# Optimization experiments

Measured on AMD Instinct MI355X. Metric: run time of the kernel, lower is better.

Reference implementation:

```python
import jax, jax.numpy as jnp
import numpy as np
import math

N_HEADS = 16
D_EMBED = 1024
D_CROSS = 768
FF_DIM = 4096
D_HEAD = D_EMBED // N_HEADS
LN_EPS = 1e-5


def layer_norm(h, g, b):
    mu = jnp.mean(h, axis=-1, keepdims=True)
    var = jnp.var(h, axis=-1, keepdims=True)
    return (h - mu) * jax.lax.rsqrt(var + LN_EPS) * g + b


def mha(q, k, v):
    # q: [B,Sq,D], k/v: [B,Skv,D] -> split heads, attend, merge
    B, Sq, _ = q.shape
    Skv = k.shape[1]
    qh = q.reshape(B, Sq, N_HEADS, D_HEAD).transpose(0, 2, 1, 3)
    kh = k.reshape(B, Skv, N_HEADS, D_HEAD).transpose(0, 2, 1, 3)
    vh = v.reshape(B, Skv, N_HEADS, D_HEAD).transpose(0, 2, 1, 3)
    scores = jnp.einsum('bhqd,bhkd->bhqk', qh, kh) / math.sqrt(D_HEAD)
    attn = jax.nn.softmax(scores, axis=-1)
    out = jnp.einsum('bhqk,bhkd->bhqd', attn, vh)
    return out.transpose(0, 2, 1, 3).reshape(B, Sq, D_EMBED)


def setup_inputs() -> dict:
    key = jax.random.key(0)
    ks = jax.random.split(key, 24)
    s = 0.02
    inp = {
        'x': jax.random.normal(ks[0], (4, 1024, D_EMBED), jnp.float32),
        'y': jax.random.normal(ks[1], (4, 77, D_CROSS), jnp.float32),
        # self-attention in_proj (d_embed -> 3*d_embed) and out_proj
        'w_qkv': jax.random.normal(ks[2], (D_EMBED, 3 * D_EMBED), jnp.float32) * s,
        'b_qkv': jnp.zeros((3 * D_EMBED,), jnp.float32),
        'w_so': jax.random.normal(ks[3], (D_EMBED, D_EMBED), jnp.float32) * s,
        'b_so': jnp.zeros((D_EMBED,), jnp.float32),
        # cross-attention projections
        'w_q': jax.random.normal(ks[4], (D_EMBED, D_EMBED), jnp.float32) * s,
        'b_q': jnp.zeros((D_EMBED,), jnp.float32),
        'w_k': jax.random.normal(ks[5], (D_CROSS, D_EMBED), jnp.float32) * s,
        'b_k': jnp.zeros((D_EMBED,), jnp.float32),
        'w_v': jax.random.normal(ks[6], (D_CROSS, D_EMBED), jnp.float32) * s,
        'b_v': jnp.zeros((D_EMBED,), jnp.float32),
        'w_co': jax.random.normal(ks[7], (D_EMBED, D_EMBED), jnp.float32) * s,
        'b_co': jnp.zeros((D_EMBED,), jnp.float32),
        # 3-layer FFN
        'w1': jax.random.normal(ks[8], (D_EMBED, FF_DIM), jnp.float32) * s,
        'b1': jnp.zeros((FF_DIM,), jnp.float32),
        'w2': jax.random.normal(ks[9], (FF_DIM, FF_DIM), jnp.float32) * s,
        'b2': jnp.zeros((FF_DIM,), jnp.float32),
        'w3': jax.random.normal(ks[10], (FF_DIM, D_EMBED), jnp.float32) * s,
        'b3': jnp.zeros((D_EMBED,), jnp.float32),
        # single shared LayerNorm (used 3 times, as in the torch module)
        'ln_g': jnp.ones((D_EMBED,), jnp.float32),
        'ln_b': jnp.zeros((D_EMBED,), jnp.float32),
    }
    return inp


def reference(x, y, w_qkv, b_qkv, w_so, b_so, w_q, b_q, w_k, b_k, w_v, b_v,
              w_co, b_co, w1, b1, w2, b2, w3, b3, ln_g, ln_b):
    # --- self attention (no causal mask) ---
    qkv = x @ w_qkv + b_qkv
    q, k, v = jnp.split(qkv, 3, axis=-1)
    sa = mha(q, k, v) @ w_so + b_so
    x = layer_norm(x + sa, ln_g, ln_b)
    # --- cross attention ---
    qc = x @ w_q + b_q
    kc = y @ w_k + b_k
    vc = y @ w_v + b_v
    ca = mha(qc, kc, vc) @ w_co + b_co
    x = layer_norm(x + ca, ln_g, ln_b)
    # --- 3-layer FFN with ReLU ---
    h = jax.nn.relu(x @ w1 + b1)
    h = jax.nn.relu(h @ w2 + b2)
    ff = h @ w3 + b3
    x = layer_norm(x + ff, ln_g, ln_b)
    return x
```

## Files before the change

### kernel.cpp

```cpp
#include <hip/hip_runtime.h>
#include <hip/hip_bf16.h>
#include <math.h>

typedef short v8s __attribute__((ext_vector_type(8)));
typedef short v4s __attribute__((ext_vector_type(4)));
typedef float v4f __attribute__((ext_vector_type(4)));

__device__ __forceinline__ unsigned short f2bf(float f) {
  union { float f; unsigned u; } a; a.f = f;
  unsigned u = a.u + 0x7fffu + ((a.u >> 16) & 1u);
  return (unsigned short)(u >> 16);
}

__device__ __forceinline__ void gld_lds16(const unsigned short* g, unsigned short* l) {
  __builtin_amdgcn_global_load_lds(
      (const __attribute__((address_space(1))) void*)g,
      (__attribute__((address_space(3))) void*)l,
      16, 0, 0);
}

#define VMCNT(n)  asm volatile("s_waitcnt vmcnt(" #n ")" ::: "memory")
#define LGKM(n)   asm volatile("s_waitcnt lgkmcnt(" #n ")" ::: "memory")

__global__ void cvt_f32_bf16(const float* __restrict__ in,
                             unsigned short* __restrict__ out, int n4) {
  int i = blockIdx.x * blockDim.x + threadIdx.x;
  if (i >= n4) return;
  float4 v = reinterpret_cast<const float4*>(in)[i];
  ushort4 o;
  o.x = f2bf(v.x); o.y = f2bf(v.y); o.z = f2bf(v.z); o.w = f2bf(v.w);
  reinterpret_cast<ushort4*>(out)[i] = o;
}

__global__ void cvt_transpose(const float* __restrict__ in,
                              unsigned short* __restrict__ out, int K, int N) {
  __shared__ float t[32][33];
  int bx = blockIdx.x, by = blockIdx.y;
  int tx = threadIdx.x, ty = threadIdx.y;
#pragma unroll
  for (int i = 0; i < 4; i++) {
    int k = by * 32 + ty + i * 8;
    t[ty + i * 8][tx] = in[(size_t)k * N + bx * 32 + tx];
  }
  __syncthreads();
#pragma unroll
  for (int i = 0; i < 4; i++) {
    int n = bx * 32 + ty + i * 8;
    out[(size_t)n * K + by * 32 + tx] = f2bf(t[tx][ty + i * 8]);
  }
}

__global__ __launch_bounds__(256)
void transpose_v(const unsigned short* __restrict__ V,
                 unsigned short* __restrict__ Vt,
                 int rowstride, int batch_rows, int Skv, int kvpad) {
  __shared__ __align__(16) unsigned short t[64][80];
  int ch = blockIdx.x, h = blockIdx.y, b = blockIdx.z;
  int tid = threadIdx.x;
  int sr = tid >> 2, sc = (tid & 3) * 16;
  int gr = ch * 64 + sr;
  v8s v0 = {}, v1 = {};
  if (gr < Skv) {
    const unsigned short* p = V + (size_t)(b * batch_rows + gr) * rowstride + h * 64 + sc;
    v0 = *(const v8s*)p; v1 = *(const v8s*)(p + 8);
  }
  *(v8s*)&t[sr][sc]     = v0;
  *(v8s*)&t[sr][sc + 8] = v1;
  __syncthreads();
  int d  = tid >> 2;
  int k0 = (tid & 3) * 16;
  unsigned short* o = Vt + ((size_t)(b * 16 + h) * 64 + d) * kvpad + ch * 64 + k0;
  v8s o0, o1;
#pragma unroll
  for (int e = 0; e < 8; e++) { o0[e] = t[k0 + e][d]; o1[e] = t[k0 + 8 + e][d]; }
  *(v8s*)o       = o0;
  *(v8s*)(o + 8) = o1;
}

#define PH_MFMA(AFR, IB, JB)                                                   \
  _Pragma("unroll")                                                            \
  for (int m = 0; m < 4; m++) {                                                \
    _Pragma("unroll")                                                          \
    for (int n = 0; n < 2; n++) {                                              \
      acc[IB + m][JB + n] = __builtin_amdgcn_mfma_f32_16x16x32_bf16(           \
          AFR[m][0], bF[n][0], acc[IB + m][JB + n], 0, 0, 0);                  \
      acc[IB + m][JB + n] = __builtin_amdgcn_mfma_f32_16x16x32_bf16(           \
          AFR[m][1], bF[n][1], acc[IB + m][JB + n], 0, 0, 0);                  \
    }                                                                          \
  }

template<bool RELU>
__global__ __launch_bounds__(512, 2)
void gemm256(const unsigned short* __restrict__ A,
             const unsigned short* __restrict__ BT,
             const float* __restrict__ bias,
             unsigned short* __restrict__ Cb,
             int M, int N, int K, int lda, int ldb) {
  __shared__ __align__(16) unsigned short lA[2][2][8192];
  __shared__ __align__(16) unsigned short lB[2][2][8192];
  int tid  = threadIdx.x;
  int lane = tid & 63;
  int wave = tid >> 6;
  int wrow = wave >> 2;
  int wcol = wave & 3;
  int quad = lane >> 4;
  int l15  = lane & 15;
  int m0 = blockIdx.y * 256;
  int n0 = blockIdx.x * 256;
  int NT = K >> 6;

  int lrow = lane >> 3;
  int swz8 = ((lane & 7) ^ lrow) << 3;
  const unsigned short* gA0 = A + (size_t)(m0 + wave * 8 + lrow) * lda + swz8;
  int rr = wave * 8 + lrow;
  int nbase = (rr >> 5) * 64 + (rr & 31);
  const unsigned short* gB0 = BT + (size_t)(n0 + nbase) * ldb + swz8;

  auto stageA = [&](int U, int h, int rlo) {
    unsigned short* d = &lA[U & 1][h][(rlo + wave * 8) * 64];
    gld_lds16(gA0 + (size_t)(h * 128 + rlo) * lda + (size_t)U * 64, d);
  };
  auto stageB = [&](int U, int hB, int q) {
    unsigned short* d = &lB[U & 1][hB][(q * 64 + wave * 8) * 64];
    gld_lds16(gB0 + (size_t)(q * 128 + hB * 32) * ldb + (size_t)U * 64, d);
  };

  int ch0 = (quad ^ (l15 & 7)) << 3;
  int ch1 = ch0 ^ 32;
  int wcol32 = wcol * 32;

  const v4f vzero = {0.f, 0.f, 0.f, 0.f};
  v4f acc[8][4];
#pragma unroll
  for (int i = 0; i < 8; i++)
#pragma unroll
    for (int j = 0; j < 4; j++) acc[i][j] = vzero;

  v8s aF0[4][2], aF1[4][2], bF[2][2];

  stageA(0, 0, 0);  stageA(0, 1, 0);
  stageB(0, 0, 0);  stageB(0, 0, 1);
  stageA(0, 0, 64); stageA(0, 1, 64);
  stageB(0, 1, 0);  stageB(0, 1, 1);
  if (NT > 1) {
    stageA(1, 0, 0);  stageA(1, 1, 0);
    stageB(1, 0, 0);  stageB(1, 0, 1);
    stageA(1, 0, 64); stageA(1, 1, 64);
    VMCNT(8);
  } else {
    VMCNT(0);
  }
  __builtin_amdgcn_s_barrier();

  for (int U = 0; U < NT; ++U) {
    int c = U & 1;
    bool tail = (U + 3 >= NT);
    const unsigned short* pA  = &lA[c][wrow][0];
    const unsigned short* pB0 = &lB[c][0][0];
    const unsigned short* pB1 = &lB[c][1][0];

#pragma unroll
    for (int m = 0; m < 4; m++) {
      int ro = (m * 16 + l15) * 64;
      aF0[m][0] = *(const v8s*)&pA[ro + ch0];
      aF0[m][1] = *(const v8s*)&pA[ro + ch1];
    }
#pragma unroll
    for (int n = 0; n < 2; n++) {
      int ro = (wcol32 + n * 16 + l15) * 64;
      bF[n][0] = *(const v8s*)&pB0[ro + ch0];
      bF[n][1] = *(const v8s*)&pB0[ro + ch1];
    }
    if (U + 1 < NT) { stageB(U + 1, 1, 0); stageB(U + 1, 1, 1); }
    LGKM(8);
    __builtin_amdgcn_s_barrier();
    LGKM(0);
    __builtin_amdgcn_sched_barrier(0);
    __builtin_amdgcn_s_setprio(1);
    PH_MFMA(aF0, 0, 0)
    __builtin_amdgcn_s_setprio(0);
    __builtin_amdgcn_s_barrier();

#pragma unroll
    for (int m = 0; m < 4; m++) {
      int ro = (64 * 64) + (m * 16 + l15) * 64;
      aF1[m][0] = *(const v8s*)&pA[ro + ch0];
      aF1[m][1] = *(const v8s*)&pA[ro + ch1];
    }
    if (U + 2 < NT) { stageA(U + 2, 0, 0); stageA(U + 2, 1, 0); }
    __builtin_amdgcn_s_barrier();
    LGKM(0);
    __builtin_amdgcn_sched_barrier(0);
    __builtin_amdgcn_s_setprio(1);
    PH_MFMA(aF1, 4, 0)
    __builtin_amdgcn_s_setprio(0);
    if (tail) { VMCNT(0); } else { VMCNT(10); }
    __builtin_amdgcn_s_barrier();

#pragma unroll
    for (int n = 0; n < 2; n++) {
      int ro = (wcol32 + n * 16 + l15) * 64;
      bF[n][0] = *(const v8s*)&pB1[ro + ch0];
      bF[n][1] = *(const v8s*)&pB1[ro + ch1];
    }
    if (U + 2 < NT) { stageB(U + 2, 0, 0); stageB(U + 2, 0, 1); }
    __builtin_amdgcn_s_barrier();
    LGKM(0);
    __builtin_amdgcn_sched_barrier(0);
    __builtin_amdgcn_s_setprio(1);
    PH_MFMA(aF1, 4, 2)
    __builtin_amdgcn_s_setprio(0);
    __builtin_amdgcn_s_barrier();

    if (U + 2 < NT) { stageA(U + 2, 0, 64); stageA(U + 2, 1, 64); }
    __builtin_amdgcn_s_barrier();
    __builtin_amdgcn_s_setprio(1);
    PH_MFMA(aF0, 0, 2)
    __builtin_amdgcn_s_setprio(0);
    if (tail) { VMCNT(0); } else { VMCNT(8); }
    __builtin_amdgcn_s_barrier();
  }

#pragma unroll
  for (int j = 0; j < 4; j++) {
    int col = n0 + wcol * 64 + (j >> 1) * 32 + (j & 1) * 16 + l15;
    float bv = bias[col];
#pragma unroll
    for (int i = 0; i < 8; i++) {
      int rb = m0 + wrow * 128 + (i >> 2) * 64 + (i & 3) * 16 + quad * 4;
#pragma unroll
      for (int r = 0; r < 4; r++) {
        int row = rb + r;
        if (row < M) {
          float v = acc[i][j][r] + bv;
          if (RELU) v = fmaxf(v, 0.f);
          Cb[(size_t)row * N + col] = f2bf(v);
        }
      }
    }
  }
}

template<bool RELU, bool OUTF, bool OUTB>
__global__ __launch_bounds__(256)
void gemm_bf16(const unsigned short* __restrict__ A,
               const unsigned short* __restrict__ BT,
               const float* __restrict__ bias,
               const float* __restrict__ bias2, int bsplit,
               float* __restrict__ Cf, float* __restrict__ Cf2,
               unsigned short* __restrict__ Cb,
               int M, int N, int Kred, int ld) {
  __shared__ __align__(16) unsigned short lA[128 * 64];
  __shared__ __align__(16) unsigned short lB[128 * 64];
  int tid  = threadIdx.x;
  int lane = tid & 63;
  int wave = tid >> 6;
  int wr = (wave >> 1) * 64;
  int wc = (wave & 1) * 64;
  int quad = lane >> 4;
  int l15  = lane & 15;
  int m0 = blockIdx.y * 128;
  int n0 = blockIdx.x * 128;
  int z  = blockIdx.z;

  const unsigned short* Az = A  + (size_t)z * Kred;
  const unsigned short* Bz = BT + (size_t)z * Kred;
  float* Cfo = z ? Cf2 : Cf;
  const float* biasz = z ? nullptr : bias;

  int srow   = tid >> 3;
  int schunk = (tid & 7) ^ (srow & 7);
  const unsigned short* gA = Az + (size_t)(m0 + srow) * ld + schunk * 8;
  const unsigned short* gB = Bz + (size_t)(n0 + srow) * ld + schunk * 8;
  unsigned short* ldsA = lA + wave * 512;
  unsigned short* ldsB = lB + wave * 512;
  const size_t rowblk = (size_t)32 * ld;

  const v4f vzero = {0.f, 0.f, 0.f, 0.f};
  v4f acc[4][4];
#pragma unroll
  for (int i = 0; i < 4; i++)
#pragma unroll
    for (int j = 0; j < 4; j++) acc[i][j] = vzero;

  for (int k0 = 0; k0 < Kred; k0 += 64) {
#pragma unroll
    for (int i = 0; i < 4; i++) {
      gld_lds16(gA + k0 + i * rowblk, ldsA + i * 2048);
      gld_lds16(gB + k0 + i * rowblk, ldsB + i * 2048);
    }
    __syncthreads();
#pragma unroll
    for (int s = 0; s < 2; s++) {
      v8s aF[4], bF[4];
#pragma unroll
      for (int i = 0; i < 4; i++)
        aF[i] = *(const v8s*)&lA[(wr + i * 16 + l15) * 64 + (((s * 4 + quad) ^ (l15 & 7)) * 8)];
#pragma unroll
      for (int j = 0; j < 4; j++)
        bF[j] = *(const v8s*)&lB[(wc + j * 16 + l15) * 64 + (((s * 4 + quad) ^ (l15 & 7)) * 8)];
#pragma unroll
      for (int i = 0; i < 4; i++)
#pragma unroll
        for (int j = 0; j < 4; j++)
          acc[i][j] = __builtin_amdgcn_mfma_f32_16x16x32_bf16(aF[i], bF[j], acc[i][j], 0, 0, 0);
    }
    __syncthreads();
  }

#pragma unroll
  for (int j = 0; j < 4; j++) {
    int col = n0 + wc + j * 16 + l15;
    float bv = 0.f;
    if (biasz) bv = (bias2 && col >= bsplit) ? bias2[col - bsplit] : biasz[col];
#pragma unroll
    for (int i = 0; i < 4; i++) {
#pragma unroll
      for (int r = 0; r < 4; r++) {
        int row = m0 + wr + i * 16 + quad * 4 + r;
        if (row < M) {
          float v = acc[i][j][r] + bv;
          if (RELU) v = fmaxf(v, 0.f);
          if (OUTF) Cfo[(size_t)row * N + col] = v;
          if (OUTB && !z) Cb[(size_t)row * N + col] = f2bf(v);
        }
      }
    }
  }
}

__global__ __launch_bounds__(256)
void attn_kernel(const unsigned short* __restrict__ Q,
                 const unsigned short* __restrict__ K,
                 const unsigned short* __restrict__ Vt,
                 unsigned short* __restrict__ O,
                 int q_rowstride, int kv_rowstride, int o_rowstride,
                 int q_batch_rows, int kv_batch_rows, int Skv, int kvpad,
                 float scale) {
  __shared__ __align__(16) unsigned short lK[64][72];
  __shared__ __align__(16) unsigned short lV[64][72];
  __shared__ __align__(16) unsigned short lP[4][16][72];
  int tid  = threadIdx.x;
  int lane = tid & 63;
  int wave = tid >> 6;
  int quad = lane >> 4;
  int l15  = lane & 15;
  int qt = blockIdx.x, h = blockIdx.y, b = blockIdx.z;

  const unsigned short* Qb  = Q  + (size_t)b * q_batch_rows * q_rowstride + h * 64;
  const unsigned short* Kb  = K  + (size_t)b * kv_batch_rows * kv_rowstride + h * 64;
  const unsigned short* Vtb = Vt + ((size_t)(b * 16 + h) * 64) * kvpad;

  v8s qf0, qf1;
  {
    const unsigned short* qr = Qb + (size_t)(qt * 64 + wave * 16 + l15) * q_rowstride + quad * 8;
    qf0 = *(const v8s*)(qr);
    qf1 = *(const v8s*)(qr + 32);
  }

  const v4f vzero = {0.f, 0.f, 0.f, 0.f};
  v4f o_acc[4];
#pragma unroll
  for (int t = 0; t < 4; t++) o_acc[t] = vzero;
  float m_r[4], l_r[4];
#pragma unroll
  for (int r = 0; r < 4; r++) { m_r[r] = -1e30f; l_r[r] = 0.f; }

  int sr = tid >> 2;
  int sc = (tid & 3) * 16;
  int nch = (Skv + 63) >> 6;

  v8s kv0 = {}, kv1 = {}, vv0, vv1;
  if (sr < Skv) {
    const unsigned short* kp = Kb + (size_t)sr * kv_rowstride + sc;
    kv0 = *(const v8s*)kp;  kv1 = *(const v8s*)(kp + 8);
  }
  {
    const unsigned short* vp = Vtb + (size_t)sr * kvpad + sc;
    vv0 = *(const v8s*)vp;  vv1 = *(const v8s*)(vp + 8);
  }

  for (int ch = 0; ch < nch; ch++) {
    int base = ch * 64;
    __builtin_amdgcn_s_barrier();
    __builtin_amdgcn_sched_barrier(0);
    *(v8s*)&lK[sr][sc]     = kv0;
    *(v8s*)&lK[sr][sc + 8] = kv1;
    {
      v4s a0 = {vv0[0], vv0[1], vv0[2], vv0[3]};
      v4s a1 = {vv0[4], vv0[5], vv0[6], vv0[7]};
      v4s a2 = {vv1[0], vv1[1], vv1[2], vv1[3]};
      v4s a3 = {vv1[4], vv1[5], vv1[6], vv1[7]};
      *(v4s*)&lV[sr][sc]      = a0;
      *(v4s*)&lV[sr][sc + 4]  = a1;
      *(v4s*)&lV[sr][sc + 8]  = a2;
      *(v4s*)&lV[sr][sc + 12] = a3;
    }
    v8s kn0 = {}, kn1 = {}, vn0 = {}, vn1 = {};
    if (ch + 1 < nch) {
      int gr2 = base + 64 + sr;
      if (gr2 < Skv) {
        const unsigned short* kp2 = Kb + (size_t)gr2 * kv_rowstride + sc;
        kn0 = *(const v8s*)kp2;  kn1 = *(const v8s*)(kp2 + 8);
      }
      const unsigned short* vp2 = Vtb + (size_t)sr * kvpad + base + 64 + sc;
      vn0 = *(const v8s*)vp2;  vn1 = *(const v8s*)(vp2 + 8);
    }
    LGKM(0);
    __builtin_amdgcn_s_barrier();
    __builtin_amdgcn_sched_barrier(0);

    float s[4][4];
#pragma unroll
    for (int t = 0; t < 4; t++) {
      v8s kf0 = *(const v8s*)&lK[t * 16 + l15][quad * 8];
      v8s kf1 = *(const v8s*)&lK[t * 16 + l15][32 + quad * 8];
      v4f sacc = vzero;
      sacc = __builtin_amdgcn_mfma_f32_16x16x32_bf16(qf0, kf0, sacc, 0, 0, 0);
      sacc = __builtin_amdgcn_mfma_f32_16x16x32_bf16(qf1, kf1, sacc, 0, 0, 0);
      int kvpos = base + t * 16 + l15;
      bool ok = kvpos < Skv;
#pragma unroll
      for (int r = 0; r < 4; r++) s[t][r] = ok ? sacc[r] * scale : -1e30f;
    }

#pragma unroll
    for (int r = 0; r < 4; r++) {
      float mx = fmaxf(fmaxf(s[0][r], s[1][r]), fmaxf(s[2][r], s[3][r]));
#pragma unroll
      for (int d = 1; d < 16; d <<= 1) mx = fmaxf(mx, __shfl_xor(mx, d));
      float mnew = fmaxf(m_r[r], mx);
      float alpha = __expf(m_r[r] - mnew);
      float sm = 0.f;
#pragma unroll
      for (int t = 0; t < 4; t++) { s[t][r] = __expf(s[t][r] - mnew); sm += s[t][r]; }
#pragma unroll
      for (int d = 1; d < 16; d <<= 1) sm += __shfl_xor(sm, d);
      l_r[r] = l_r[r] * alpha + sm;
      m_r[r] = mnew;
#pragma unroll
      for (int t = 0; t < 4; t++) o_acc[t][r] *= alpha;
    }

#pragma unroll
    for (int t = 0; t < 4; t++)
#pragma unroll
      for (int r = 0; r < 4; r++)
        lP[wave][quad * 4 + r][t * 16 + l15] = f2bf(s[t][r]);
    v8s pf0 = *(const v8s*)&lP[wave][l15][quad * 8];
    v8s pf1 = *(const v8s*)&lP[wave][l15][32 + quad * 8];
#pragma unroll
    for (int t = 0; t < 4; t++) {
      v8s vf0 = *(const v8s*)&lV[t * 16 + l15][quad * 8];
      v8s vf1 = *(const v8s*)&lV[t * 16 + l15][32 + quad * 8];
      o_acc[t] = __builtin_amdgcn_mfma_f32_16x16x32_bf16(pf0, vf0, o_acc[t], 0, 0, 0);
      o_acc[t] = __builtin_amdgcn_mfma_f32_16x16x32_bf16(pf1, vf1, o_acc[t], 0, 0, 0);
    }

    kv0 = kn0; kv1 = kn1; vv0 = vn0; vv1 = vn1;
  }

  int orow0 = b * q_batch_rows + qt * 64 + wave * 16;
#pragma unroll
  for (int t = 0; t < 4; t++) {
#pragma unroll
    for (int r = 0; r < 4; r++) {
      float v = o_acc[t][r] / l_r[r];
      O[(size_t)(orow0 + quad * 4 + r) * o_rowstride + h * 64 + t * 16 + l15] = f2bf(v);
    }
  }
}

__global__ __launch_bounds__(256)
void ln_kernel(const float* base, const float* __restrict__ delta,
               const float* __restrict__ delta2,
               const float* __restrict__ g, const float* __restrict__ bb,
               float* outf, unsigned short* __restrict__ outb) {
  __shared__ float red[8];
  int row = blockIdx.x;
  int tid = threadIdx.x;
  float4 vb = ((const float4*)(base  + (size_t)row * 1024))[tid];
  float4 vd = ((const float4*)(delta + (size_t)row * 1024))[tid];
  float v0 = vb.x + vd.x, v1 = vb.y + vd.y, v2 = vb.z + vd.z, v3 = vb.w + vd.w;
  if (delta2) {
    float4 v2d = ((const float4*)(delta2 + (size_t)row * 1024))[tid];
    v0 += v2d.x; v1 += v2d.y; v2 += v2d.z; v3 += v2d.w;
  }
  float s = v0 + v1 + v2 + v3;
  float q = v0 * v0 + v1 * v1 + v2 * v2 + v3 * v3;
#pragma unroll
  for (int d = 1; d < 64; d <<= 1) { s += __shfl_xor(s, d); q += __shfl_xor(q, d); }
  int wave = tid >> 6, lane = tid & 63;
  if (lane == 0) { red[wave] = s; red[4 + wave] = q; }
  __syncthreads();
  s = red[0] + red[1] + red[2] + red[3];
  q = red[4] + red[5] + red[6] + red[7];
  float mean = s * (1.f / 1024.f);
  float var  = q * (1.f / 1024.f) - mean * mean;
  float rstd = rsqrtf(var + 1e-5f);
  float4 gg  = ((const float4*)g)[tid];
  float4 bv  = ((const float4*)bb)[tid];
  float o0 = (v0 - mean) * rstd * gg.x + bv.x;
  float o1 = (v1 - mean) * rstd * gg.y + bv.y;
  float o2 = (v2 - mean) * rstd * gg.z + bv.z;
  float o3 = (v3 - mean) * rstd * gg.w + bv.w;
  if (outf) {
    float4 o; o.x = o0; o.y = o1; o.z = o2; o.w = o3;
    ((float4*)(outf + (size_t)row * 1024))[tid] = o;
  }
  if (outb) {
    ushort4 u; u.x = f2bf(o0); u.y = f2bf(o1); u.z = f2bf(o2); u.w = f2bf(o3);
    ((ushort4*)(outb + (size_t)row * 1024))[tid] = u;
  }
}

extern "C" void kernel_launch(void* const* d_in, const int* in_sizes, int n_in,
                              void* d_out, int out_size, void* d_ws, size_t ws_size,
                              hipStream_t stream) {
  const float* x     = (const float*)d_in[0];
  const float* y     = (const float*)d_in[1];
  const float* w_qkv = (const float*)d_in[2];
  const float* b_qkv = (const float*)d_in[3];
  const float* w_so  = (const float*)d_in[4];
  const float* b_so  = (const float*)d_in[5];
  const float* w_q   = (const float*)d_in[6];
  const float* b_q   = (const float*)d_in[7];
  const float* w_k   = (const float*)d_in[8];
  const float* b_k   = (const float*)d_in[9];
  const float* w_v   = (const float*)d_in[10];
  const float* b_v   = (const float*)d_in[11];
  const float* w_co  = (const float*)d_in[12];
  const float* b_co  = (const float*)d_in[13];
  const float* w1    = (const float*)d_in[14];
  const float* b1    = (const float*)d_in[15];
  const float* w2    = (const float*)d_in[16];
  const float* b2    = (const float*)d_in[17];
  const float* w3    = (const float*)d_in[18];
  const float* b3    = (const float*)d_in[19];
  const float* ln_g  = (const float*)d_in[20];
  const float* ln_b  = (const float*)d_in[21];

  char* ws = (char*)d_ws;
  auto US = [&](size_t off) { return (unsigned short*)(ws + off); };
  auto FP = [&](size_t off) { return (float*)(ws + off); };

  constexpr size_t o_wqkv = 0;
  constexpr size_t o_wso  = o_wqkv + 3072ull * 1024 * 2;
  constexpr size_t o_wq   = o_wso  + 1024ull * 1024 * 2;
  constexpr size_t o_wk   = o_wq   + 1024ull * 1024 * 2;
  constexpr size_t o_wv   = o_wk   + 1024ull * 768 * 2;
  constexpr size_t o_wco  = o_wv   + 1024ull * 768 * 2;
  constexpr size_t o_w1   = o_wco  + 1024ull * 1024 * 2;
  constexpr size_t o_w2   = o_w1   + 4096ull * 1024 * 2;
  constexpr size_t o_w3   = o_w2   + 4096ull * 4096 * 2;
  constexpr size_t o_xf   = o_w3   + 1024ull * 4096 * 2;
  constexpr size_t o_xbf  = o_xf   + 4096ull * 1024 * 4;
  constexpr size_t o_ybf  = o_xbf  + 4096ull * 1024 * 2;
  constexpr size_t o_dlt  = o_ybf  + 308ull * 768 * 2;
  constexpr size_t o_R1   = o_dlt  + 4096ull * 1024 * 4;
  constexpr size_t o_attn = o_R1   + 4096ull * 3072 * 2;
  constexpr size_t o_R2   = o_attn + 4096ull * 1024 * 2;
  constexpr size_t o_qc  = o_R1;
  constexpr size_t o_kc  = o_R1 + 4096ull * 1024 * 2;
  constexpr size_t o_h1  = o_R1;
  constexpr size_t o_h2  = o_R2;
  constexpr size_t o_dlt2 = o_R1;
  constexpr size_t o_vtS = o_R2;
  constexpr size_t o_vtC = o_R2 + 4ull * 16 * 64 * 1024 * 2;

  dim3 tb(32, 8);
  cvt_transpose<<<dim3(96, 32),  tb, 0, stream>>>(w_qkv, US(o_wqkv), 1024, 3072);
  cvt_transpose<<<dim3(32, 32),  tb, 0, stream>>>(w_so,  US(o_wso),  1024, 1024);
  cvt_transpose<<<dim3(32, 32),  tb, 0, stream>>>(w_q,   US(o_wq),   1024, 1024);
  cvt_transpose<<<dim3(32, 24),  tb, 0, stream>>>(w_k,   US(o_wk),   768,  1024);
  cvt_transpose<<<dim3(32, 24),  tb, 0, stream>>>(w_v,   US(o_wv),   768,  1024);
  cvt_transpose<<<dim3(32, 32),  tb, 0, stream>>>(w_co,  US(o_wco),  1024, 1024);
  cvt_transpose<<<dim3(128, 32), tb, 0, stream>>>(w1,    US(o_w1),   1024, 4096);
  cvt_transpose<<<dim3(128, 128),tb, 0, stream>>>(w2,    US(o_w2),   4096, 4096);
  cvt_transpose<<<dim3(32, 128), tb, 0, stream>>>(w3,    US(o_w3),   4096, 1024);

  cvt_f32_bf16<<<4096, 256, 0, stream>>>(x, US(o_xbf), 4096 * 1024 / 4);
  cvt_f32_bf16<<<231, 256, 0, stream>>>(y, US(o_ybf), 4 * 77 * 768 / 4);

  gemm256<false><<<dim3(12, 16), 512, 0, stream>>>(
      US(o_xbf), US(o_wqkv), b_qkv, US(o_R1), 4096, 3072, 1024, 1024, 1024);
  transpose_v<<<dim3(16, 16, 4), 256, 0, stream>>>(
      US(o_R1) + 2048, US(o_vtS), 3072, 1024, 1024, 1024);
  attn_kernel<<<dim3(16, 16, 4), 256, 0, stream>>>(
      US(o_R1), US(o_R1) + 1024, US(o_vtS), US(o_attn),
      3072, 3072, 1024, 1024, 1024, 1024, 1024, 0.125f);
  gemm_bf16<false, true, false><<<dim3(8, 32, 2), 256, 0, stream>>>(
      US(o_attn), US(o_wso), b_so, nullptr, 0,
      FP(o_dlt), FP(o_dlt2), nullptr, 4096, 1024, 512, 1024);
  ln_kernel<<<4096, 256, 0, stream>>>(x, FP(o_dlt), FP(o_dlt2), ln_g, ln_b,
                                      FP(o_xf), US(o_xbf));

  gemm_bf16<false, false, true><<<dim3(8, 32, 1), 256, 0, stream>>>(
      US(o_xbf), US(o_wq), b_q, nullptr, 0,
      nullptr, nullptr, US(o_qc), 4096, 1024, 1024, 1024);
  gemm_bf16<false, false, true><<<dim3(16, 3, 1), 256, 0, stream>>>(
      US(o_ybf), US(o_wk), b_k, b_v, 1024,
      nullptr, nullptr, US(o_kc), 308, 2048, 768, 768);
  transpose_v<<<dim3(2, 16, 4), 256, 0, stream>>>(
      US(o_kc) + 1024, US(o_vtC), 2048, 77, 77, 128);
  attn_kernel<<<dim3(16, 16, 4), 256, 0, stream>>>(
      US(o_qc), US(o_kc), US(o_vtC), US(o_attn),
      1024, 2048, 1024, 1024, 77, 77, 128, 0.125f);
  gemm_bf16<false, true, false><<<dim3(8, 32, 2), 256, 0, stream>>>(
      US(o_attn), US(o_wco), b_co, nullptr, 0,
      FP(o_dlt), FP(o_dlt2), nullptr, 4096, 1024, 512, 1024);
  ln_kernel<<<4096, 256, 0, stream>>>(FP(o_xf), FP(o_dlt), FP(o_dlt2), ln_g, ln_b,
                                      FP(o_xf), US(o_xbf));

  gemm256<true><<<dim3(16, 16), 512, 0, stream>>>(
      US(o_xbf), US(o_w1), b1, US(o_h1), 4096, 4096, 1024, 1024, 1024);
  gemm256<true><<<dim3(16, 16), 512, 0, stream>>>(
      US(o_h1), US(o_w2), b2, US(o_h2), 4096, 4096, 4096, 4096, 4096);
  gemm_bf16<false, true, false><<<dim3(8, 32, 2), 256, 0, stream>>>(
      US(o_h2), US(o_w3), b3, nullptr, 0,
      FP(o_dlt), FP(o_dlt2), nullptr, 4096, 1024, 2048, 4096);
  ln_kernel<<<4096, 256, 0, stream>>>(FP(o_xf), FP(o_dlt), FP(o_dlt2), ln_g, ln_b,
                                      (float*)d_out, nullptr);
}
```

Before: 735.9 us.

## Restructure gemm256 main loop into two K-half phases with simpler LDS layout

Replaces the four-phase ping-pong schedule of the 256x256 GEMM with two phases per K-tile, each splitting the tile by K-halves of 32 and issuing a full 8x4 MFMA block per wave. The LDS staging layout is changed to store 32-element K-halves per row with a new XOR swizzle, and the wave-to-output mapping becomes contiguous 16-row/16-col fragments. The aim is fewer barriers and simpler prefetch accounting. In exchange it drops the set-priority interleaving and holds more fragment registers live, which may reduce latency hiding or raise register pressure.

```diff
diff --git a/kernel.cpp b/kernel.cpp
--- a/kernel.cpp
+++ b/kernel.cpp
@@ -76,18 +76,6 @@
   *(v8s*)o       = o0;
   *(v8s*)(o + 8) = o1;
 }
-
-#define PH_MFMA(AFR, IB, JB)                                                   \
-  _Pragma("unroll")                                                            \
-  for (int m = 0; m < 4; m++) {                                                \
-    _Pragma("unroll")                                                          \
-    for (int n = 0; n < 2; n++) {                                              \
-      acc[IB + m][JB + n] = __builtin_amdgcn_mfma_f32_16x16x32_bf16(           \
-          AFR[m][0], bF[n][0], acc[IB + m][JB + n], 0, 0, 0);                  \
-      acc[IB + m][JB + n] = __builtin_amdgcn_mfma_f32_16x16x32_bf16(           \
-          AFR[m][1], bF[n][1], acc[IB + m][JB + n], 0, 0, 0);                  \
-    }                                                                          \
-  }
 
 template<bool RELU>
 __global__ __launch_bounds__(512, 2)
@@ -109,25 +97,28 @@
   int n0 = blockIdx.x * 256;
   int NT = K >> 6;
 
-  int lrow = lane >> 3;
-  int swz8 = ((lane & 7) ^ lrow) << 3;
-  const unsigned short* gA0 = A + (size_t)(m0 + wave * 8 + lrow) * lda + swz8;
-  int rr = wave * 8 + lrow;
-  int nbase = (rr >> 5) * 64 + (rr & 31);
-  const unsigned short* gB0 = BT + (size_t)(n0 + nbase) * ldb + swz8;
-
-  auto stageA = [&](int U, int h, int rlo) {
-    unsigned short* d = &lA[U & 1][h][(rlo + wave * 8) * 64];
-    gld_lds16(gA0 + (size_t)(h * 128 + rlo) * lda + (size_t)U * 64, d);
+  int srow  = wave * 16 + (lane >> 2);
+  int scol8 = ((lane & 3) ^ ((lane >> 3) & 3)) << 3;
+  const unsigned short* gA0 = A  + (size_t)(m0 + srow) * lda + scol8;
+  const unsigned short* gB0 = BT + (size_t)(n0 + srow) * ldb + scol8;
+
+  auto stA = [&](int U, int kh) {
+    unsigned short* d = &lA[U & 1][kh][wave * 512];
+    const unsigned short* s = gA0 + (size_t)U * 64 + kh * 32;
+    gld_lds16(s, d);
+    gld_lds16(s + (size_t)128 * lda, d + 4096);
   };
-  auto stageB = [&](int U, int hB, int q) {
-    unsigned short* d = &lB[U & 1][hB][(q * 64 + wave * 8) * 64];
-    gld_lds16(gB0 + (size_t)(q * 128 + hB * 32) * ldb + (size_t)U * 64, d);
+  auto stB = [&](int U, int kh) {
+    unsigned short* d = &lB[U & 1][kh][wave * 512];
+    const unsigned short* s = gB0 + (size_t)U * 64 + kh * 32;
+    gld_lds16(s, d);
+    gld_lds16(s + (size_t)128 * ldb, d + 4096);
   };
 
-  int ch0 = (quad ^ (l15 & 7)) << 3;
-  int ch1 = ch0 ^ 32;
-  int wcol32 = wcol * 32;
+  int rsw  = (l15 >> 1) & 3;
+  int cho  = (quad ^ rsw) << 3;
+  int aOff = (wrow * 128 + l15) * 32 + cho;
+  int bOff = (wcol * 64  + l15) * 32 + cho;
 
   const v4f vzero = {0.f, 0.f, 0.f, 0.f};
   v4f acc[8][4];
@@ -136,98 +127,65 @@
 #pragma unroll
     for (int j = 0; j < 4; j++) acc[i][j] = vzero;
 
-  v8s aF0[4][2], aF1[4][2], bF[2][2];
-
-  stageA(0, 0, 0);  stageA(0, 1, 0);
-  stageB(0, 0, 0);  stageB(0, 0, 1);
-  stageA(0, 0, 64); stageA(0, 1, 64);
-  stageB(0, 1, 0);  stageB(0, 1, 1);
-  if (NT > 1) {
-    stageA(1, 0, 0);  stageA(1, 1, 0);
-    stageB(1, 0, 0);  stageB(1, 0, 1);
-    stageA(1, 0, 64); stageA(1, 1, 64);
-    VMCNT(8);
-  } else {
-    VMCNT(0);
-  }
+  stA(0, 0); stB(0, 0);
+  stA(0, 1); stB(0, 1);
+  if (NT > 1) { stA(1, 0); stB(1, 0); VMCNT(4); }
+  else        { VMCNT(0); }
   __builtin_amdgcn_s_barrier();
+  __builtin_amdgcn_sched_barrier(0);
 
   for (int U = 0; U < NT; ++U) {
     int c = U & 1;
-    bool tail = (U + 3 >= NT);
-    const unsigned short* pA  = &lA[c][wrow][0];
-    const unsigned short* pB0 = &lB[c][0][0];
-    const unsigned short* pB1 = &lB[c][1][0];
-
-#pragma unroll
-    for (int m = 0; m < 4; m++) {
-      int ro = (m * 16 + l15) * 64;
-      aF0[m][0] = *(const v8s*)&pA[ro + ch0];
-      aF0[m][1] = *(const v8s*)&pA[ro + ch1];
-    }
-#pragma unroll
-    for (int n = 0; n < 2; n++) {
-      int ro = (wcol32 + n * 16 + l15) * 64;
-      bF[n][0] = *(const v8s*)&pB0[ro + ch0];
-      bF[n][1] = *(const v8s*)&pB0[ro + ch1];
-    }
-    if (U + 1 < NT) { stageB(U + 1, 1, 0); stageB(U + 1, 1, 1); }
-    LGKM(8);
-    __builtin_amdgcn_s_barrier();
+    v8s aF[8], bFr[4];
+
+    if (U + 1 < NT) { stA(U + 1, 1); stB(U + 1, 1); }
+
+    {
+      const unsigned short* pA = &lA[c][0][0];
+      const unsigned short* pB = &lB[c][0][0];
+#pragma unroll
+      for (int m = 0; m < 8; m++) aF[m]  = *(const v8s*)&pA[aOff + m * 512];
+#pragma unroll
+      for (int n = 0; n < 4; n++) bFr[n] = *(const v8s*)&pB[bOff + n * 512];
+#pragma unroll
+      for (int m = 0; m < 8; m++)
+#pragma unroll
+        for (int n = 0; n < 4; n++)
+          acc[m][n] = __builtin_amdgcn_mfma_f32_16x16x32_bf16(aF[m], bFr[n], acc[m][n], 0, 0, 0);
+    }
     LGKM(0);
     __builtin_amdgcn_sched_barrier(0);
-    __builtin_amdgcn_s_setprio(1);
-    PH_MFMA(aF0, 0, 0)
-    __builtin_amdgcn_s_setprio(0);
     __builtin_amdgcn_s_barrier();
 
-#pragma unroll
-    for (int m = 0; m < 4; m++) {
-      int ro = (64 * 64) + (m * 16 + l15) * 64;
-      aF1[m][0] = *(const v8s*)&pA[ro + ch0];
-      aF1[m][1] = *(const v8s*)&pA[ro + ch1];
-    }
-    if (U + 2 < NT) { stageA(U + 2, 0, 0); stageA(U + 2, 1, 0); }
-    __builtin_amdgcn_s_barrier();
+    if (U + 2 < NT) { stA(U + 2, 0); stB(U + 2, 0); }
+
+    {
+      const unsigned short* pA = &lA[c][1][0];
+      const unsigned short* pB = &lB[c][1][0];
+#pragma unroll
+      for (int m = 0; m < 8; m++) aF[m]  = *(const v8s*)&pA[aOff + m * 512];
+#pragma unroll
+      for (int n = 0; n < 4; n++) bFr[n] = *(const v8s*)&pB[bOff + n * 512];
+#pragma unroll
+      for (int m = 0; m < 8; m++)
+#pragma unroll
+        for (int n = 0; n < 4; n++)
+          acc[m][n] = __builtin_amdgcn_mfma_f32_16x16x32_bf16(aF[m], bFr[n], acc[m][n], 0, 0, 0);
+    }
     LGKM(0);
     __builtin_amdgcn_sched_barrier(0);
-    __builtin_amdgcn_s_setprio(1);
-    PH_MFMA(aF1, 4, 0)
-    __builtin_amdgcn_s_setprio(0);
-    if (tail) { VMCNT(0); } else { VMCNT(10); }
+    if (U + 2 < NT) { VMCNT(4); } else { VMCNT(0); }
     __builtin_amdgcn_s_barrier();
-
-#pragma unroll
-    for (int n = 0; n < 2; n++) {
-      int ro = (wcol32 + n * 16 + l15) * 64;
-      bF[n][0] = *(const v8s*)&pB1[ro + ch0];
-      bF[n][1] = *(const v8s*)&pB1[ro + ch1];
-    }
-    if (U + 2 < NT) { stageB(U + 2, 0, 0); stageB(U + 2, 0, 1); }
-    __builtin_amdgcn_s_barrier();
-    LGKM(0);
     __builtin_amdgcn_sched_barrier(0);
-    __builtin_amdgcn_s_setprio(1);
-    PH_MFMA(aF1, 4, 2)
-    __builtin_amdgcn_s_setprio(0);
-    __builtin_amdgcn_s_barrier();
-
-    if (U + 2 < NT) { stageA(U + 2, 0, 64); stageA(U + 2, 1, 64); }
-    __builtin_amdgcn_s_barrier();
-    __builtin_amdgcn_s_setprio(1);
-    PH_MFMA(aF0, 0, 2)
-    __builtin_amdgcn_s_setprio(0);
-    if (tail) { VMCNT(0); } else { VMCNT(8); }
-    __builtin_amdgcn_s_barrier();
   }
 
 #pragma unroll
   for (int j = 0; j < 4; j++) {
-    int col = n0 + wcol * 64 + (j >> 1) * 32 + (j & 1) * 16 + l15;
+    int col = n0 + wcol * 64 + j * 16 + l15;
     float bv = bias[col];
 #pragma unroll
     for (int i = 0; i < 8; i++) {
-      int rb = m0 + wrow * 128 + (i >> 2) * 64 + (i & 3) * 16 + quad * 4;
+      int rb = m0 + wrow * 128 + i * 16 + quad * 4;
 #pragma unroll
       for (int r = 0; r < 4; r++) {
         int row = rb + r;
```

New measurement: 743.6 us. No clear change (+1.0%).
